# Kernel optimization log

Measured on AMD Instinct MI355X. Metric: run time of the kernel, lower is better.

## Reference

```python
import jax, jax.numpy as jnp
import numpy as np
from jax import lax

NUM_CLASSES = 80
TOPK = 13
ALPHA = 1.0
BETA = 6.0
EPS = 1e-9
P = 150000
N = 256


def _make_boxes(key, n, scale):
    k1, k2 = jax.random.split(key)
    xy = jax.random.uniform(k1, (n, 2), dtype=jnp.float32) * scale
    wh = jax.random.uniform(k2, (n, 2), dtype=jnp.float32) * (0.2 * scale) + 1.0
    return jnp.concatenate([xy, xy + wh], axis=-1)  # valid x1y1x2y2


def setup_inputs() -> dict:
    key = jax.random.key(0)
    k1, k2, k3, k4 = jax.random.split(key, 4)
    cls_pred = jax.random.uniform(k1, (P, NUM_CLASSES), dtype=jnp.float32)
    bbox_pred = _make_boxes(k2, P, 640.0)
    bbox_gt = _make_boxes(k3, N, 640.0)
    # FG labels are > 0 (code indexes cls_pred[label-1])
    label_gt = jax.random.randint(k4, (N, 1), 1, NUM_CLASSES + 1, dtype=jnp.int32)
    return {"cls_pred": cls_pred, "bbox_pred": bbox_pred, "label_gt": label_gt, "bbox_gt": bbox_gt}


def _ious(bbox1, bbox2, eps=EPS):
    # bbox1: (N,4) gt, bbox2: (P,4) pred -> (N,P)
    b1 = bbox1[:, None, :]
    b2 = bbox2[None, :, :]
    x1y1 = jnp.maximum(b1[..., 0:2], b2[..., 0:2])
    x2y2 = jnp.minimum(b1[..., 2:4], b2[..., 2:4])
    inter = jnp.clip(x2y2 - x1y1, 0.0).prod(-1)
    area1 = jnp.clip(b1[..., 2:4] - b1[..., 0:2], 0.0).prod(-1)
    area2 = jnp.clip(b2[..., 2:4] - b2[..., 0:2], 0.0).prod(-1)
    return inter / (area1 + area2 - inter + eps)


def _metrics_topk(metrics, topk, eps=EPS):
    n, num_priors = metrics.shape
    topk_vals, topk_idxs = lax.top_k(metrics, topk)  # (N,k)
    keep = topk_vals.max(axis=-1, keepdims=True) > eps
    topk_idxs = jnp.where(keep, topk_idxs, 0)
    rows = jnp.arange(n)[:, None]
    counts = jnp.zeros((n, num_priors), jnp.int32).at[rows, topk_idxs].add(1)
    is_in_topk = jnp.where(counts > 1, 0, counts)
    return is_in_topk.astype(metrics.dtype)


def reference(cls_pred, bbox_pred, label_gt, bbox_gt):
    num_priors, num_classes = cls_pred.shape
    n_gt = bbox_gt.shape[0]
    ious = _ious(bbox_gt, bbox_pred)  # (N,P)
    lbl = label_gt.reshape(-1).astype(jnp.int32)  # (N,)
    bbox_cls_scores = jnp.take(cls_pred.T, lbl - 1, axis=0)  # (N,P)
    alignment_metrics = jnp.power(bbox_cls_scores, ALPHA) * jnp.power(ious, BETA)
    mask_positive = _metrics_topk(alignment_metrics, TOPK)  # (N,P) float 0/1
    mask_positive_sum = mask_positive.sum(axis=0)  # (P,)
    # conflict resolution: priors claimed by >1 gt go to the max-iou gt.
    # Applying unconditionally equals the torch data-dependent branch.
    is_max_iou = (jnp.arange(n_gt)[:, None] == ious.argmax(axis=0)[None, :]).astype(ious.dtype)
    mask_positive = jnp.where(mask_positive_sum[None, :] > 1, is_max_iou, mask_positive)
    mask_positive_sum = mask_positive.sum(axis=0)
    assigned_gt_index = mask_positive.argmax(axis=0)  # (P,)
    assigned_labels = lbl[assigned_gt_index]  # (P,)
    assigned_cls = jax.nn.one_hot(assigned_labels - 1, num_classes, dtype=jnp.int32)
    assigned_bboxes = bbox_gt[assigned_gt_index]  # (P,4)
    assigned_labels = jnp.where(mask_positive_sum > 0, assigned_labels, 0)
    return (assigned_gt_index, assigned_labels, assigned_cls, assigned_bboxes)
```

## Files before the change

### kernel.cpp

```cpp
#include <hip/hip_runtime.h>

#define TOPK 13
#define NCLS 80
#define EPSF 1e-9f
#define NSEG 32
#define GPB  8
#define CAP3 512
#define MCAP (64 * TOPK)

__global__ __launch_bounds__(256) void sortgt(const int* __restrict__ lbl,
                                              int* __restrict__ gorder, int N) {
    __shared__ int key[256];
    int t = threadIdx.x;
    key[t] = (t < N) ? ((lbl[t] << 8) | t) : 0x7FFFFFFF;
    __syncthreads();
    for (int k = 2; k <= 256; k <<= 1) {
        for (int j = k >> 1; j >= 1; j >>= 1) {
            int ixj = t ^ j;
            if (ixj > t) {
                int a = key[t], b = key[ixj];
                bool up = ((t & k) == 0);
                if (up ? (a > b) : (a < b)) { key[t] = b; key[ixj] = a; }
            }
            __syncthreads();
        }
    }
    if (t < N) gorder[t] = key[t] & 0xFF;
}

__global__ __launch_bounds__(512, 4) void phaseA1(const float* __restrict__ cls,
                                                  const float4* __restrict__ bboxp,
                                                  const float4* __restrict__ bboxg,
                                                  const int* __restrict__ lbl,
                                                  const int* __restrict__ gorder,
                                                  float2* __restrict__ cand,
                                                  int P, int N, int seglen) {
#pragma clang fp contract(off)
    const int s = blockIdx.x, tile = blockIdx.y, t = threadIdx.x;
    const int wv = t >> 6, lane = t & 63;
    const int pstart = s * seglen;
    int pend = pstart + seglen; if (pend > P) pend = P;

    __shared__ int pbuf[GPB][CAP3];
    __shared__ float2 mbuf[GPB][MCAP];
    __shared__ int ctr[GPB];

    float4 gb[GPB];
#pragma unroll
    for (int j = 0; j < GPB; j++) {
        int gi8 = tile * GPB + j;
        int gj = (gi8 < N) ? gorder[gi8] : -1;
        gb[j] = (gj >= 0) ? bboxg[gj] : make_float4(0.f, 0.f, 0.f, 0.f);
    }
    if (t < GPB) ctr[t] = 0;
    __syncthreads();

    bool first = true;
    for (int p = pstart + t; p < pend; p += 512) {
        float4 pb = bboxp[p];
        bool force = first && (t < 16);
        first = false;
#pragma unroll
        for (int j = 0; j < GPB; j++) {
            float dx = fminf(gb[j].z, pb.z) - fmaxf(gb[j].x, pb.x);
            float dy = fminf(gb[j].w, pb.w) - fmaxf(gb[j].y, pb.y);
            bool want = ((dx > 0.0f) && (dy > 0.0f)) || force;
            if (want) {
                int slot = atomicAdd(&ctr[j], 1);
                if (slot < CAP3) pbuf[j][slot] = p;
            }
        }
    }
    __syncthreads();

    const int gi8 = tile * GPB + wv;
    const bool myValid = gi8 < N;
    const int gj = myValid ? gorder[gi8] : 0;
    const float4 gbw = bboxg[gj];
    const float gaw = fmaxf(gbw.z - gbw.x, 0.0f) * fmaxf(gbw.w - gbw.y, 0.0f);
    const int cidx = lbl[gj] - 1;
    const int rawtotal = ctr[wv];

    float v[TOPK]; int id[TOPK];
#pragma unroll
    for (int k = 0; k < TOPK; k++) { v[k] = -1.0f; id[k] = 0x7FFFFFFF; }

    auto ins = [&](float m, int p) {
        bool b12 = (m > v[TOPK - 1]) || (m == v[TOPK - 1] && p < id[TOPK - 1]);
        if (b12) {
#pragma unroll
            for (int k = TOPK - 1; k >= 1; k--) {
                bool a = (m > v[k - 1]) || (m == v[k - 1] && p < id[k - 1]);
                bool b = (m > v[k]) || (m == v[k] && p < id[k]);
                float nv = a ? v[k - 1] : (b ? m : v[k]);
                int   ni = a ? id[k - 1] : (b ? p : id[k]);
                v[k] = nv; id[k] = ni;
            }
            bool a0 = (m > v[0]) || (m == v[0] && p < id[0]);
            if (a0) { v[0] = m; id[0] = p; }
        }
    };

    if (rawtotal <= CAP3) {
        for (int e = lane; e < rawtotal; e += 64) {
            int p = pbuf[wv][e];
            float4 pb = bboxp[p];
            float sc = cls[(size_t)p * NCLS + cidx];
            float pa = fmaxf(pb.z - pb.x, 0.0f) * fmaxf(pb.w - pb.y, 0.0f);
            float xx1 = fmaxf(gbw.x, pb.x), yy1 = fmaxf(gbw.y, pb.y);
            float xx2 = fminf(gbw.z, pb.z), yy2 = fminf(gbw.w, pb.w);
            float inter = fmaxf(xx2 - xx1, 0.0f) * fmaxf(yy2 - yy1, 0.0f);
            float iou = inter / (((gaw + pa) - inter) + EPSF);
            float i2 = iou * iou;
            float m = sc * ((i2 * i2) * i2);
            ins(m, p);
        }
    } else if (myValid) {
        for (int p = pstart + lane; p < pend; p += 64) {
            float4 pb = bboxp[p];
            float sc = cls[(size_t)p * NCLS + cidx];
            float pa = fmaxf(pb.z - pb.x, 0.0f) * fmaxf(pb.w - pb.y, 0.0f);
            float xx1 = fmaxf(gbw.x, pb.x), yy1 = fmaxf(gbw.y, pb.y);
            float xx2 = fminf(gbw.z, pb.z), yy2 = fminf(gbw.w, pb.w);
            float inter = fmaxf(xx2 - xx1, 0.0f) * fmaxf(yy2 - yy1, 0.0f);
            float iou = inter / (((gaw + pa) - inter) + EPSF);
            float i2 = iou * iou;
            float m = sc * ((i2 * i2) * i2);
            ins(m, p);
        }
    }

    float2* wl = mbuf[wv];
#pragma unroll
    for (int k = 0; k < TOPK; k++)
        wl[lane * TOPK + k] = make_float2(v[k], __int_as_float(id[k]));
    __syncthreads();
    for (int str = 32; str >= 1; str >>= 1) {
        if (lane < str) {
            float2 merged[TOPK];
            int a = 0, b = 0;
            const int ba = lane * TOPK, bb = (lane + str) * TOPK;
#pragma unroll
            for (int k = 0; k < TOPK; k++) {
                float2 fa = wl[ba + a], fb = wl[bb + b];
                int ia = __float_as_int(fa.y), ib = __float_as_int(fb.y);
                bool takeA = (fa.x > fb.x) || (fa.x == fb.x && ia < ib);
                merged[k] = takeA ? fa : fb;
                a += takeA; b += !takeA;
            }
#pragma unroll
            for (int k = 0; k < TOPK; k++) wl[ba + k] = merged[k];
        }
        __syncthreads();
    }
    if (lane < TOPK && myValid)
        cand[((size_t)gj * NSEG + s) * TOPK + lane] = wl[lane];
}

__global__ __launch_bounds__(512) void phaseA2(const float2* __restrict__ cand,
                                               int* __restrict__ count,
                                               int* __restrict__ firstg) {
    const int g = blockIdx.x;
    const int t = threadIdx.x;
    const int M = NSEG * TOPK;
    __shared__ float cv[512];
    __shared__ int   ci[512];
    if (t < M) {
        float2 e = cand[(size_t)g * M + t];
        cv[t] = e.x; ci[t] = __float_as_int(e.y);
    } else {
        cv[t] = -1.0f; ci[t] = 0x7FFFFFFF;
    }
    __syncthreads();
    for (int k = 2; k <= 512; k <<= 1) {
        for (int j = k >> 1; j >= 1; j >>= 1) {
            int ixj = t ^ j;
            if (ixj > t) {
                float va = cv[t], vb = cv[ixj];
                int   ia = ci[t], ib = ci[ixj];
                bool aBeforeB = (va > vb) || (va == vb && ia < ib);
                bool dirFwd = ((t & k) == 0);
                bool doswap = dirFwd ? !aBeforeB : aBeforeB;
                if (doswap) { cv[t] = vb; ci[t] = ib; cv[ixj] = va; ci[ixj] = ia; }
            }
            __syncthreads();
        }
    }
    if (t < TOPK && cv[0] > EPSF) {
        int pi = ci[t];
        atomicAdd(&count[pi], 1);
        atomicMin(&firstg[pi], g);
    }
}

__global__ __launch_bounds__(256) void phaseCF(const float4* __restrict__ bboxp,
                                               const float4* __restrict__ bboxg,
                                               const int* __restrict__ lbl,
                                               const int* __restrict__ count,
                                               const int* __restrict__ firstg,
                                               float* __restrict__ out0,
                                               float* __restrict__ out1,
                                               float4* __restrict__ outcls4,
                                               float4* __restrict__ outbox4, int P, int N) {
#pragma clang fp contract(off)
    __shared__ float4 gbS[256];
    __shared__ int glS[256];
    __shared__ int gil[256];
    __shared__ int clsl[256];
    int t = threadIdx.x;
    if (t < N) { gbS[t] = bboxg[t]; glS[t] = lbl[t]; }
    __syncthreads();
    int p0 = blockIdx.x * 256;
    int nloc = P - p0; if (nloc > 256) nloc = 256;
    if (t < nloc) {
        int p = p0 + t;
        int cnt = count[p];
        int gi = 0, pos = 0;
        if (cnt == 1) { gi = firstg[p]; pos = 1; }
        else if (cnt > 1) {
            float4 pb = bboxp[p];
            float pa = fmaxf(pb.z - pb.x, 0.0f) * fmaxf(pb.w - pb.y, 0.0f);
            float best = -1.0f;
            for (int g = 0; g < N; g++) {
                float4 g4 = gbS[g];
                float gar = fmaxf(g4.z - g4.x, 0.0f) * fmaxf(g4.w - g4.y, 0.0f);
                float xx1 = fmaxf(g4.x, pb.x), yy1 = fmaxf(g4.y, pb.y);
                float xx2 = fminf(g4.z, pb.z), yy2 = fminf(g4.w, pb.w);
                float inter = fmaxf(xx2 - xx1, 0.0f) * fmaxf(yy2 - yy1, 0.0f);
                float iou = inter / (((gar + pa) - inter) + EPSF);
                if (iou > best) { best = iou; gi = g; }
            }
            pos = 1;
        }
        out0[p] = (float)gi;
        out1[p] = pos ? (float)glS[gi] : 0.0f;
        gil[t] = gi;
        clsl[t] = glS[gi] - 1;
        outbox4[p] = gbS[gi];
    }
    __syncthreads();
    for (int f = t; f < nloc * 20; f += 256) {
        int pl = f / 20, q = f - pl * 20;
        int cl = clsl[pl], c0 = q * 4;
        float4 vv = make_float4(c0 == cl ? 1.0f : 0.0f, c0 + 1 == cl ? 1.0f : 0.0f,
                                c0 + 2 == cl ? 1.0f : 0.0f, c0 + 3 == cl ? 1.0f : 0.0f);
        outcls4[(size_t)p0 * 20 + f] = vv;
    }
}

__global__ __launch_bounds__(256) void phaseC1(const float4* __restrict__ bboxp,
                                               const float4* __restrict__ bboxg,
                                               const int* __restrict__ lbl,
                                               const int* __restrict__ count,
                                               const int* __restrict__ firstg,
                                               float* __restrict__ out0,
                                               float* __restrict__ out1, int P, int N) {
#pragma clang fp contract(off)
    __shared__ float4 gbS[256];
    __shared__ int glS[256];
    if (threadIdx.x < (unsigned)N) {
        gbS[threadIdx.x] = bboxg[threadIdx.x];
        glS[threadIdx.x] = lbl[threadIdx.x];
    }
    __syncthreads();
    int p = blockIdx.x * 256 + threadIdx.x;
    if (p >= P) return;
    int cnt = count[p];
    int gi = 0, pos = 0;
    if (cnt == 1) { gi = firstg[p]; pos = 1; }
    else if (cnt > 1) {
        float4 pb = bboxp[p];
        float pa = fmaxf(pb.z - pb.x, 0.0f) * fmaxf(pb.w - pb.y, 0.0f);
        float best = -1.0f;
        for (int g = 0; g < N; g++) {
            float4 g4 = gbS[g];
            float gar = fmaxf(g4.z - g4.x, 0.0f) * fmaxf(g4.w - g4.y, 0.0f);
            float xx1 = fmaxf(g4.x, pb.x), yy1 = fmaxf(g4.y, pb.y);
            float xx2 = fminf(g4.z, pb.z), yy2 = fminf(g4.w, pb.w);
            float inter = fmaxf(xx2 - xx1, 0.0f) * fmaxf(yy2 - yy1, 0.0f);
            float iou = inter / (((gar + pa) - inter) + EPSF);
            if (iou > best) { best = iou; gi = g; }
        }
        pos = 1;
    }
    out0[p] = (float)gi;
    out1[p] = pos ? (float)glS[gi] : 0.0f;
}

__global__ __launch_bounds__(256) void phaseC2(const float4* __restrict__ bboxg,
                                               const int* __restrict__ lbl,
                                               const float* __restrict__ out0,
                                               float* __restrict__ outcls,
                                               float* __restrict__ outbox, int P, int N) {
    __shared__ float gbb[256 * 4];
    __shared__ int glS[256];
    __shared__ int clsl[256];
    __shared__ int gil[256];
    int tid = threadIdx.x;
    if (tid < N) {
        float4 b = bboxg[tid];
        gbb[tid * 4 + 0] = b.x; gbb[tid * 4 + 1] = b.y;
        gbb[tid * 4 + 2] = b.z; gbb[tid * 4 + 3] = b.w;
        glS[tid] = lbl[tid];
    }
    __syncthreads();
    int p0 = blockIdx.x * 256;
    int nloc = P - p0; if (nloc > 256) nloc = 256;
    if (tid < nloc) {
        int gi = (int)out0[p0 + tid];
        gil[tid] = gi;
        clsl[tid] = glS[gi] - 1;
    }
    __syncthreads();
    for (int f = tid; f < nloc * NCLS; f += 256) {
        int pl = f / NCLS;
        int c  = f - pl * NCLS;
        outcls[(size_t)p0 * NCLS + f] = (c == clsl[pl]) ? 1.0f : 0.0f;
    }
    for (int f = tid; f < nloc * 4; f += 256) {
        int pl = f >> 2, k = f & 3;
        outbox[(size_t)p0 * 4 + f] = gbb[gil[pl] * 4 + k];
    }
}

extern "C" void kernel_launch(void* const* d_in, const int* in_sizes, int n_in,
                              void* d_out, int out_size, void* d_ws, size_t ws_size,
                              hipStream_t stream) {
    const float* cls_pred  = (const float*)d_in[0];
    const float* bbox_pred = (const float*)d_in[1];
    const int*   label_gt  = (const int*)d_in[2];
    const float* bbox_gt   = (const float*)d_in[3];
    int P = in_sizes[1] / 4;
    int N = in_sizes[3] / 4;

    float* out    = (float*)d_out;
    float* out0   = out;
    float* out1   = out + (size_t)P;
    float* outcls = out + (size_t)2 * P;
    float* outbox = out + (size_t)82 * P;

    int pb = (P + 255) / 256;
    int seglen = (P + NSEG - 1) / NSEG;
    int gtiles = (N + GPB - 1) / GPB;
    dim3 gridA1(NSEG, gtiles);
    size_t candBytes = (size_t)N * NSEG * TOPK * sizeof(float2);
    size_t needWs = (size_t)P * 8 + candBytes + (size_t)N * 4 + 64;

    if (ws_size >= needWs) {
        int*    count  = (int*)d_ws;
        int*    firstg = count + P;
        float2* cand   = (float2*)(firstg + P);
        int*    gorder = (int*)((char*)cand + candBytes);

        hipMemsetAsync(count, 0, (size_t)P * sizeof(int), stream);
        hipMemsetAsync(firstg, 0x7F, (size_t)P * sizeof(int), stream);
        sortgt<<<1, 256, 0, stream>>>(label_gt, gorder, N);
        phaseA1<<<gridA1, 512, 0, stream>>>(cls_pred, (const float4*)bbox_pred,
                                            (const float4*)bbox_gt, label_gt, gorder,
                                            cand, P, N, seglen);
        phaseA2<<<N, 512, 0, stream>>>(cand, count, firstg);
        phaseCF<<<pb, 256, 0, stream>>>((const float4*)bbox_pred, (const float4*)bbox_gt,
                                        label_gt, count, firstg, out0, out1,
                                        (float4*)outcls, (float4*)outbox, P, N);
    } else {
        int*    count  = (int*)outbox;
        int*    firstg = ((int*)outbox) + P;
        float2* cand   = (float2*)(((int*)outbox) + 2 * (size_t)P);
        int*    gorder = (int*)((char*)cand + candBytes);

        hipMemsetAsync(count, 0, (size_t)P * sizeof(int), stream);
        hipMemsetAsync(firstg, 0x7F, (size_t)P * sizeof(int), stream);
        sortgt<<<1, 256, 0, stream>>>(label_gt, gorder, N);
        phaseA1<<<gridA1, 512, 0, stream>>>(cls_pred, (const float4*)bbox_pred,
                                            (const float4*)bbox_gt, label_gt, gorder,
                                            cand, P, N, seglen);
        phaseA2<<<N, 512, 0, stream>>>(cand, count, firstg);
        phaseC1<<<pb, 256, 0, stream>>>((const float4*)bbox_pred, (const float4*)bbox_gt,
                                        label_gt, count, firstg, out0, out1, P, N);
        phaseC2<<<pb, 256, 0, stream>>>((const float4*)bbox_gt, label_gt, out0,
                                        outcls, outbox, P, N);
    }
}
```

Measured before the change: 221.5 us.

## Fuse final top-k merge into phaseA1 via last-block counter and merge setup kernels

Removes the phaseA2 kernel: each segment block bumps a per-gt done counter, and the last block to finish merges all segment candidates with a register insertion sort and wave-level merge, then performs the count/firstg atomics. The two memsets and the gt sort are folded into one setup kernel, NSEG drops to 24, pbuf aliases mbuf to cut shared memory (occupancy hint raised to 6), and the candidate loads are unrolled by four. It removes launches and the bitonic sort pass, at the cost of a serialized tail merge in one wave and reliance on threadfence ordering. The merge loop also drops its __syncthreads, relying on intra-wave lockstep execution.

```diff
diff --git a/kernel.cpp b/kernel.cpp
--- a/kernel.cpp
+++ b/kernel.cpp
@@ -3,37 +3,71 @@
 #define TOPK 13
 #define NCLS 80
 #define EPSF 1e-9f
-#define NSEG 32
+#define NSEG 24
 #define GPB  8
 #define CAP3 512
 #define MCAP (64 * TOPK)
 
-__global__ __launch_bounds__(256) void sortgt(const int* __restrict__ lbl,
-                                              int* __restrict__ gorder, int N) {
-    __shared__ int key[256];
+#define INS(vv, ii, m, p)                                                      \
+    do {                                                                       \
+        bool b12_ = (m > vv[TOPK - 1]) || (m == vv[TOPK - 1] && p < ii[TOPK - 1]); \
+        if (b12_) {                                                            \
+            _Pragma("unroll")                                                  \
+            for (int k_ = TOPK - 1; k_ >= 1; k_--) {                           \
+                bool a_ = (m > vv[k_ - 1]) || (m == vv[k_ - 1] && p < ii[k_ - 1]); \
+                bool b_ = (m > vv[k_]) || (m == vv[k_] && p < ii[k_]);         \
+                float nv_ = a_ ? vv[k_ - 1] : (b_ ? m : vv[k_]);               \
+                int   ni_ = a_ ? ii[k_ - 1] : (b_ ? p : ii[k_]);               \
+                vv[k_] = nv_; ii[k_] = ni_;                                    \
+            }                                                                  \
+            bool a0_ = (m > vv[0]) || (m == vv[0] && p < ii[0]);               \
+            if (a0_) { vv[0] = m; ii[0] = p; }                                 \
+        }                                                                      \
+    } while (0)
+
+__global__ __launch_bounds__(256) void setup(const int* __restrict__ lbl,
+                                             int* __restrict__ count,
+                                             int* __restrict__ firstg,
+                                             int* __restrict__ done,
+                                             int* __restrict__ gorder, int P, int N) {
     int t = threadIdx.x;
-    key[t] = (t < N) ? ((lbl[t] << 8) | t) : 0x7FFFFFFF;
-    __syncthreads();
-    for (int k = 2; k <= 256; k <<= 1) {
-        for (int j = k >> 1; j >= 1; j >>= 1) {
-            int ixj = t ^ j;
-            if (ixj > t) {
-                int a = key[t], b = key[ixj];
-                bool up = ((t & k) == 0);
-                if (up ? (a > b) : (a < b)) { key[t] = b; key[ixj] = a; }
-            }
-            __syncthreads();
-        }
-    }
-    if (t < N) gorder[t] = key[t] & 0xFF;
-}
-
-__global__ __launch_bounds__(512, 4) void phaseA1(const float* __restrict__ cls,
+    if (blockIdx.x == 0) {
+        __shared__ int key[256];
+        if (t < N) done[t] = 0;
+        key[t] = (t < N) ? ((lbl[t] << 8) | t) : 0x7FFFFFFF;
+        __syncthreads();
+        for (int k = 2; k <= 256; k <<= 1) {
+            for (int j = k >> 1; j >= 1; j >>= 1) {
+                int ixj = t ^ j;
+                if (ixj > t) {
+                    int a = key[t], b = key[ixj];
+                    bool up = ((t & k) == 0);
+                    if (up ? (a > b) : (a < b)) { key[t] = b; key[ixj] = a; }
+                }
+                __syncthreads();
+            }
+        }
+        if (t < N) gorder[t] = key[t] & 0xFF;
+    } else {
+        int base = (blockIdx.x - 1) * 1024 + t * 4;
+        if (base + 3 < P) {
+            *(int4*)&count[base]  = make_int4(0, 0, 0, 0);
+            *(int4*)&firstg[base] = make_int4(0x7FFFFFFF, 0x7FFFFFFF, 0x7FFFFFFF, 0x7FFFFFFF);
+        } else {
+            for (int i = base; i < P; i++) { count[i] = 0; firstg[i] = 0x7FFFFFFF; }
+        }
+    }
+}
+
+__global__ __launch_bounds__(512, 6) void phaseA1(const float* __restrict__ cls,
                                                   const float4* __restrict__ bboxp,
                                                   const float4* __restrict__ bboxg,
                                                   const int* __restrict__ lbl,
                                                   const int* __restrict__ gorder,
                                                   float2* __restrict__ cand,
+                                                  int* __restrict__ done,
+                                                  int* __restrict__ count,
+                                                  int* __restrict__ firstg,
                                                   int P, int N, int seglen) {
 #pragma clang fp contract(off)
     const int s = blockIdx.x, tile = blockIdx.y, t = threadIdx.x;
@@ -41,9 +75,9 @@
     const int pstart = s * seglen;
     int pend = pstart + seglen; if (pend > P) pend = P;
 
-    __shared__ int pbuf[GPB][CAP3];
     __shared__ float2 mbuf[GPB][MCAP];
     __shared__ int ctr[GPB];
+    int* pbuf = (int*)&mbuf[0][0];
 
     float4 gb[GPB];
 #pragma unroll
@@ -55,22 +89,32 @@
     if (t < GPB) ctr[t] = 0;
     __syncthreads();
 
-    bool first = true;
-    for (int p = pstart + t; p < pend; p += 512) {
-        float4 pb = bboxp[p];
-        bool force = first && (t < 16);
-        first = false;
+    auto testapp = [&](float4 pb, int p, bool force) {
 #pragma unroll
         for (int j = 0; j < GPB; j++) {
             float dx = fminf(gb[j].z, pb.z) - fmaxf(gb[j].x, pb.x);
             float dy = fminf(gb[j].w, pb.w) - fmaxf(gb[j].y, pb.y);
-            bool want = ((dx > 0.0f) && (dy > 0.0f)) || force;
+            bool want = (fminf(dx, dy) > 0.0f) || force;
             if (want) {
                 int slot = atomicAdd(&ctr[j], 1);
-                if (slot < CAP3) pbuf[j][slot] = p;
-            }
-        }
-    }
+                if (slot < CAP3) pbuf[j * CAP3 + slot] = p;
+            }
+        }
+    };
+
+    int p = pstart + t;
+    if (p < pend) { testapp(bboxp[p], p, t < 16); p += 512; }
+    for (; p + 1536 < pend; p += 2048) {
+        float4 pb0 = bboxp[p];
+        float4 pb1 = bboxp[p + 512];
+        float4 pb2 = bboxp[p + 1024];
+        float4 pb3 = bboxp[p + 1536];
+        testapp(pb0, p, false);
+        testapp(pb1, p + 512, false);
+        testapp(pb2, p + 1024, false);
+        testapp(pb3, p + 1536, false);
+    }
+    for (; p < pend; p += 512) testapp(bboxp[p], p, false);
     __syncthreads();
 
     const int gi8 = tile * GPB + wv;
@@ -85,27 +129,11 @@
 #pragma unroll
     for (int k = 0; k < TOPK; k++) { v[k] = -1.0f; id[k] = 0x7FFFFFFF; }
 
-    auto ins = [&](float m, int p) {
-        bool b12 = (m > v[TOPK - 1]) || (m == v[TOPK - 1] && p < id[TOPK - 1]);
-        if (b12) {
-#pragma unroll
-            for (int k = TOPK - 1; k >= 1; k--) {
-                bool a = (m > v[k - 1]) || (m == v[k - 1] && p < id[k - 1]);
-                bool b = (m > v[k]) || (m == v[k] && p < id[k]);
-                float nv = a ? v[k - 1] : (b ? m : v[k]);
-                int   ni = a ? id[k - 1] : (b ? p : id[k]);
-                v[k] = nv; id[k] = ni;
-            }
-            bool a0 = (m > v[0]) || (m == v[0] && p < id[0]);
-            if (a0) { v[0] = m; id[0] = p; }
-        }
-    };
-
     if (rawtotal <= CAP3) {
         for (int e = lane; e < rawtotal; e += 64) {
-            int p = pbuf[wv][e];
-            float4 pb = bboxp[p];
-            float sc = cls[(size_t)p * NCLS + cidx];
+            int pp = pbuf[wv * CAP3 + e];
+            float4 pb = bboxp[pp];
+            float sc = cls[(size_t)pp * NCLS + cidx];
             float pa = fmaxf(pb.z - pb.x, 0.0f) * fmaxf(pb.w - pb.y, 0.0f);
             float xx1 = fmaxf(gbw.x, pb.x), yy1 = fmaxf(gbw.y, pb.y);
             float xx2 = fminf(gbw.z, pb.z), yy2 = fminf(gbw.w, pb.w);
@@ -113,12 +141,12 @@
             float iou = inter / (((gaw + pa) - inter) + EPSF);
             float i2 = iou * iou;
             float m = sc * ((i2 * i2) * i2);
-            ins(m, p);
+            INS(v, id, m, pp);
         }
     } else if (myValid) {
-        for (int p = pstart + lane; p < pend; p += 64) {
-            float4 pb = bboxp[p];
-            float sc = cls[(size_t)p * NCLS + cidx];
+        for (int pp = pstart + lane; pp < pend; pp += 64) {
+            float4 pb = bboxp[pp];
+            float sc = cls[(size_t)pp * NCLS + cidx];
             float pa = fmaxf(pb.z - pb.x, 0.0f) * fmaxf(pb.w - pb.y, 0.0f);
             float xx1 = fmaxf(gbw.x, pb.x), yy1 = fmaxf(gbw.y, pb.y);
             float xx2 = fminf(gbw.z, pb.z), yy2 = fminf(gbw.w, pb.w);
@@ -126,15 +154,15 @@
             float iou = inter / (((gaw + pa) - inter) + EPSF);
             float i2 = iou * iou;
             float m = sc * ((i2 * i2) * i2);
-            ins(m, p);
-        }
-    }
-
-    float2* wl = mbuf[wv];
+            INS(v, id, m, pp);
+        }
+    }
+    __syncthreads();
+
+    float2* wl = &mbuf[wv][0];
 #pragma unroll
     for (int k = 0; k < TOPK; k++)
         wl[lane * TOPK + k] = make_float2(v[k], __int_as_float(id[k]));
-    __syncthreads();
     for (int str = 32; str >= 1; str >>= 1) {
         if (lane < str) {
             float2 merged[TOPK];
@@ -151,45 +179,53 @@
 #pragma unroll
             for (int k = 0; k < TOPK; k++) wl[ba + k] = merged[k];
         }
-        __syncthreads();
     }
     if (lane < TOPK && myValid)
         cand[((size_t)gj * NSEG + s) * TOPK + lane] = wl[lane];
-}
-
-__global__ __launch_bounds__(512) void phaseA2(const float2* __restrict__ cand,
-                                               int* __restrict__ count,
-                                               int* __restrict__ firstg) {
-    const int g = blockIdx.x;
-    const int t = threadIdx.x;
-    const int M = NSEG * TOPK;
-    __shared__ float cv[512];
-    __shared__ int   ci[512];
-    if (t < M) {
-        float2 e = cand[(size_t)g * M + t];
-        cv[t] = e.x; ci[t] = __float_as_int(e.y);
-    } else {
-        cv[t] = -1.0f; ci[t] = 0x7FFFFFFF;
-    }
-    __syncthreads();
-    for (int k = 2; k <= 512; k <<= 1) {
-        for (int j = k >> 1; j >= 1; j >>= 1) {
-            int ixj = t ^ j;
-            if (ixj > t) {
-                float va = cv[t], vb = cv[ixj];
-                int   ia = ci[t], ib = ci[ixj];
-                bool aBeforeB = (va > vb) || (va == vb && ia < ib);
-                bool dirFwd = ((t & k) == 0);
-                bool doswap = dirFwd ? !aBeforeB : aBeforeB;
-                if (doswap) { cv[t] = vb; ci[t] = ib; cv[ixj] = va; ci[ixj] = ia; }
-            }
-            __syncthreads();
-        }
-    }
-    if (t < TOPK && cv[0] > EPSF) {
-        int pi = ci[t];
-        atomicAdd(&count[pi], 1);
-        atomicMin(&firstg[pi], g);
+
+    if (myValid) {
+        __threadfence();
+        int old = 0;
+        if (lane == 0) old = atomicAdd(&done[gj], 1);
+        old = __shfl(old, 0);
+        if (old == NSEG - 1) {
+            __threadfence();
+            float v2[TOPK]; int id2[TOPK];
+#pragma unroll
+            for (int k = 0; k < TOPK; k++) { v2[k] = -1.0f; id2[k] = 0x7FFFFFFF; }
+            const float2* cg = cand + (size_t)gj * NSEG * TOPK;
+            for (int e = lane; e < NSEG * TOPK; e += 64) {
+                float2 E = cg[e];
+                int pp = __float_as_int(E.y);
+                float m = E.x;
+                INS(v2, id2, m, pp);
+            }
+#pragma unroll
+            for (int k = 0; k < TOPK; k++)
+                wl[lane * TOPK + k] = make_float2(v2[k], __int_as_float(id2[k]));
+            for (int str = 32; str >= 1; str >>= 1) {
+                if (lane < str) {
+                    float2 merged[TOPK];
+                    int a = 0, b = 0;
+                    const int ba = lane * TOPK, bb = (lane + str) * TOPK;
+#pragma unroll
+                    for (int k = 0; k < TOPK; k++) {
+                        float2 fa = wl[ba + a], fb = wl[bb + b];
+                        int ia = __float_as_int(fa.y), ib = __float_as_int(fb.y);
+                        bool takeA = (fa.x > fb.x) || (fa.x == fb.x && ia < ib);
+                        merged[k] = takeA ? fa : fb;
+                        a += takeA; b += !takeA;
+                    }
+#pragma unroll
+                    for (int k = 0; k < TOPK; k++) wl[ba + k] = merged[k];
+                }
+            }
+            if (lane < TOPK && wl[0].x > EPSF) {
+                int pi = __float_as_int(wl[lane].y);
+                atomicAdd(&count[pi], 1);
+                atomicMin(&firstg[pi], gj);
+            }
+        }
     }
 }
 
@@ -205,7 +241,6 @@
 #pragma clang fp contract(off)
     __shared__ float4 gbS[256];
     __shared__ int glS[256];
-    __shared__ int gil[256];
     __shared__ int clsl[256];
     int t = threadIdx.x;
     if (t < N) { gbS[t] = bboxg[t]; glS[t] = lbl[t]; }
@@ -234,7 +269,6 @@
         }
         out0[p] = (float)gi;
         out1[p] = pos ? (float)glS[gi] : 0.0f;
-        gil[t] = gi;
         clsl[t] = glS[gi] - 1;
         outbox4[p] = gbS[gi];
     }
@@ -343,22 +377,21 @@
     int seglen = (P + NSEG - 1) / NSEG;
     int gtiles = (N + GPB - 1) / GPB;
     dim3 gridA1(NSEG, gtiles);
+    int setupBlocks = 1 + (P + 1023) / 1024;
     size_t candBytes = (size_t)N * NSEG * TOPK * sizeof(float2);
-    size_t needWs = (size_t)P * 8 + candBytes + (size_t)N * 4 + 64;
+    size_t needWs = (size_t)P * 8 + candBytes + (size_t)N * 8 + 64;
 
     if (ws_size >= needWs) {
         int*    count  = (int*)d_ws;
         int*    firstg = count + P;
         float2* cand   = (float2*)(firstg + P);
-        int*    gorder = (int*)((char*)cand + candBytes);
-
-        hipMemsetAsync(count, 0, (size_t)P * sizeof(int), stream);
-        hipMemsetAsync(firstg, 0x7F, (size_t)P * sizeof(int), stream);
-        sortgt<<<1, 256, 0, stream>>>(label_gt, gorder, N);
+        int*    done   = (int*)((char*)cand + candBytes);
+        int*    gorder = done + N;
+
+        setup<<<setupBlocks, 256, 0, stream>>>(label_gt, count, firstg, done, gorder, P, N);
         phaseA1<<<gridA1, 512, 0, stream>>>(cls_pred, (const float4*)bbox_pred,
                                             (const float4*)bbox_gt, label_gt, gorder,
-                                            cand, P, N, seglen);
-        phaseA2<<<N, 512, 0, stream>>>(cand, count, firstg);
+                                            cand, done, count, firstg, P, N, seglen);
         phaseCF<<<pb, 256, 0, stream>>>((const float4*)bbox_pred, (const float4*)bbox_gt,
                                         label_gt, count, firstg, out0, out1,
                                         (float4*)outcls, (float4*)outbox, P, N);
@@ -366,15 +399,13 @@
         int*    count  = (int*)outbox;
         int*    firstg = ((int*)outbox) + P;
         float2* cand   = (float2*)(((int*)outbox) + 2 * (size_t)P);
-        int*    gorder = (int*)((char*)cand + candBytes);
-
-        hipMemsetAsync(count, 0, (size_t)P * sizeof(int), stream);
-        hipMemsetAsync(firstg, 0x7F, (size_t)P * sizeof(int), stream);
-        sortgt<<<1, 256, 0, stream>>>(label_gt, gorder, N);
+        int*    done   = (int*)((char*)cand + candBytes);
+        int*    gorder = done + N;
+
+        setup<<<setupBlocks, 256, 0, stream>>>(label_gt, count, firstg, done, gorder, P, N);
         phaseA1<<<gridA1, 512, 0, stream>>>(cls_pred, (const float4*)bbox_pred,
                                             (const float4*)bbox_gt, label_gt, gorder,
-                                            cand, P, N, seglen);
-        phaseA2<<<N, 512, 0, stream>>>(cand, count, firstg);
+                                            cand, done, count, firstg, P, N, seglen);
         phaseC1<<<pb, 256, 0, stream>>>((const float4*)bbox_pred, (const float4*)bbox_gt,
                                         label_gt, count, firstg, out0, out1, P, N);
         phaseC2<<<pb, 256, 0, stream>>>((const float4*)bbox_gt, label_gt, out0,
```

Measured after the change: 449.3 us. 2.03x slower.
